# Optimization experiments

Hardware: AMD Instinct MI355X
Metric: run time of the kernel (lower is better)

Reference implementation:

```python
import jax, jax.numpy as jnp
import numpy as np

N = 100_000      # nodes
E = 400_000      # edges
POS = 3          # pos_dim
F = 128          # feats_dim (kernel_dim)
M = 16           # m_dim
FE = 16          # fourier_features
EIN = 2 * F + 2 * FE + 1   # 289 edge mlp input
EHID = 2 * EIN             # 578
NIN = F + M                # 144
NHID = 2 * F               # 256
EPS = 1e-5


def _ln(x, g, b):
    m = x.mean(-1, keepdims=True)
    v = ((x - m) ** 2).mean(-1, keepdims=True)
    return (x - m) * jax.lax.rsqrt(v + EPS) * g + b


def setup_inputs() -> dict:
    key = jax.random.key(0)
    ks = jax.random.split(key, 8)

    def xav(k, i, o):
        return jax.random.normal(k, (i, o), jnp.float32) * np.float32(np.sqrt(2.0 / (i + o)))

    x = jax.random.normal(ks[0], (N, POS + F), jnp.float32)
    edge_index = jax.random.randint(ks[1], (2, E), 0, N, dtype=jnp.int64)
    return {
        "x": x,
        "edge_index": edge_index,
        "e_w1": xav(ks[2], EIN, EHID), "e_b1": jnp.zeros((EHID,), jnp.float32),
        "e_w2": xav(ks[3], EHID, M),   "e_b2": jnp.zeros((M,), jnp.float32),
        "en1_g": jnp.ones((M,), jnp.float32), "en1_b": jnp.zeros((M,), jnp.float32),
        "en2_g": jnp.ones((M,), jnp.float32), "en2_b": jnp.zeros((M,), jnp.float32),
        "nn1_g": jnp.ones((F,), jnp.float32), "nn1_b": jnp.zeros((F,), jnp.float32),
        "n_w1": xav(ks[4], NIN, NHID), "n_b1": jnp.zeros((NHID,), jnp.float32),
        "n_w2": xav(ks[5], NHID, F),   "n_b2": jnp.zeros((F,), jnp.float32),
        "nn2_g": jnp.ones((F,), jnp.float32), "nn2_b": jnp.zeros((F,), jnp.float32),
    }


def reference(x, edge_index, e_w1, e_b1, e_w2, e_b2, en1_g, en1_b, en2_g, en2_b,
              nn1_g, nn1_b, n_w1, n_b1, n_w2, n_b2, nn2_g, nn2_b):
    coors, feats = x[:, :POS], x[:, POS:]
    src, dst = edge_index[0], edge_index[1]  # x_j = feats[src], x_i = feats[dst]

    rel = coors[src] - coors[dst]                      # [E,3]
    d = (rel ** 2).sum(-1, keepdims=True)              # [E,1] squared distance
    scales = jnp.asarray(2.0, jnp.float32) ** jnp.arange(FE)
    ds = d / scales                                    # [E,FE]
    edge_attr = jnp.concatenate([jnp.sin(ds), jnp.cos(ds), d], -1)  # [E,2*FE+1]

    # edge MLP + LayerNorm (message)
    m = jnp.concatenate([feats[dst], feats[src], edge_attr], -1)    # [E,EIN]
    m = jax.nn.silu(m @ e_w1 + e_b1)
    m = jax.nn.silu(m @ e_w2 + e_b2)                                # [E,M]
    m = _ln(m, en1_g, en1_b)

    # scatter-add to target nodes, then LayerNorm
    m_i = jax.ops.segment_sum(m, dst, num_segments=N)               # [N,M]
    m_i = _ln(m_i, en2_g, en2_b)

    # node update MLP with residual
    h = jnp.concatenate([_ln(feats, nn1_g, nn1_b), m_i], -1)        # [N,NIN]
    h = jax.nn.silu(h @ n_w1 + n_b1)
    h = h @ n_w2 + n_b2
    h = _ln(h, nn2_g, nn2_b)
    out = feats + h
    return jnp.concatenate([coors, out], -1)                        # [N,POS+F]
```

## Files before the change

### kernel.cpp

```cpp
#include <hip/hip_runtime.h>
#include <math.h>

#define N_NODES 100000
#define N_EDGES 400000
#define POSD 3
#define F 128
#define M 16
#define EIN 289
#define EHID 578
#define NIN 144
#define NHID 256
#define ROW 131
#define LNEPS 1e-5f

#define KP 320
#define KPA 328
#define NP 640
#define EPB 32
#define NSLICE 10
#define NTW 5
#define HIDP 640
#define HIDPA 648

#define NPB2 80
#define NK1 160
#define NK1P 168
#define NSL2 5
#define NHIDP 264

typedef _Float16 half8 __attribute__((ext_vector_type(8)));
typedef _Float16 half4 __attribute__((ext_vector_type(4)));
typedef float f32x4 __attribute__((ext_vector_type(4)));

__device__ __forceinline__ float silu_f(float v) { return v / (1.f + __expf(-v)); }

__global__ __launch_bounds__(256) void prep_feats(
    const float* __restrict__ x, _Float16* __restrict__ feats)
{
    long long i = (long long)blockIdx.x * 256 + threadIdx.x;
    if (i < (long long)N_NODES * F) {
        int n = (int)(i >> 7), k = (int)(i & 127);
        feats[i] = (_Float16)x[(long long)n * ROW + POSD + k];
    }
}

__global__ __launch_bounds__(256) void prep_weights(
    const float* __restrict__ w1, const float* __restrict__ w2,
    _Float16* __restrict__ w1ks, _Float16* __restrict__ w2t)
{
    long long idx = (long long)blockIdx.x * 256 + threadIdx.x;
    const long long n1 = (long long)NSLICE * NP * 32;
    if (idx < n1) {
        int s   = (int)(idx / (NP * 32));
        int rem = (int)(idx - (long long)s * (NP * 32));
        int c   = rem >> 5;
        int kk  = rem & 31;
        int k   = s * 32 + kk;
        float v = (k < EIN && c < EHID) ? w1[(long long)k * EHID + c] : 0.f;
        w1ks[idx] = (_Float16)v;
    } else {
        long long j = idx - n1;
        if (j < (long long)M * HIDP) {
            int oc = (int)(j / HIDP);
            int k  = (int)(j - (long long)oc * HIDP);
            float v = (k < EHID) ? w2[(long long)k * M + oc] : 0.f;
            w2t[j] = (_Float16)v;
        }
    }
}

__global__ __launch_bounds__(256) void prep_weights_node(
    const float* __restrict__ w1, const float* __restrict__ w2,
    _Float16* __restrict__ w1ks2, _Float16* __restrict__ w2ks)
{
    int idx = blockIdx.x * 256 + threadIdx.x;
    const int n1 = NSL2 * 256 * 32;
    if (idx < n1) {
        int s = idx >> 13, rem = idx & 8191;
        int c = rem >> 5, kk = rem & 31;
        int k = s * 32 + kk;
        w1ks2[idx] = (_Float16)((k < NIN) ? w1[k * NHID + c] : 0.f);
    } else if (idx < n1 + 8 * 128 * 32) {
        int j = idx - n1;
        int s = j >> 12, rem = j & 4095;
        int c = rem >> 5, kk = rem & 31;
        int k = s * 32 + kk;
        w2ks[j] = (_Float16)w2[k * F + c];
    }
}

__global__ __launch_bounds__(512, 4) void edge_kernel(
    const _Float16* __restrict__ feats, const float* __restrict__ x,
    const int* __restrict__ ei,
    const _Float16* __restrict__ w1ks, const float* __restrict__ b1,
    const _Float16* __restrict__ w2t, const float* __restrict__ b2,
    const float* __restrict__ g1, const float* __restrict__ bb1,
    float* __restrict__ m_i)
{
    __shared__ __align__(16) _Float16 smem[EPB * HIDPA];
    _Float16* lds_A = smem;
    _Float16* lds_H = smem;
    __shared__ float part[4][EPB][M];
    __shared__ int   src_s[EPB], dst_s[EPB];
    __shared__ float d_s[EPB];

    const int t    = threadIdx.x;
    const int lane = t & 63;
    const int wv   = t >> 6;
    const int cl16 = lane & 15;
    const int h4   = lane >> 4;
    const long long ebase = (long long)blockIdx.x * EPB;

    if (t < EPB) {
        int s = ei[ebase + t];
        int d = ei[(long long)N_EDGES + ebase + t];
        src_s[t] = s; dst_s[t] = d;
        float dx = x[(long long)s*ROW+0] - x[(long long)d*ROW+0];
        float dy = x[(long long)s*ROW+1] - x[(long long)d*ROW+1];
        float dz = x[(long long)s*ROW+2] - x[(long long)d*ROW+2];
        d_s[t] = dx*dx + dy*dy + dz*dz;
    }
    __syncthreads();

    for (int i = t; i < EPB * 32; i += 512) {
        int row = i >> 5, g = i & 31;
        int node = (g < 16) ? dst_s[row] : src_s[row];
        half8 v = *(const half8*)(feats + (long long)node * F + ((g & 15) << 3));
        *(half8*)(lds_A + row * KPA + (g << 3)) = v;
    }
    for (int i = t; i < EPB * 64; i += 512) {
        int row = i >> 6, j = i & 63;
        float v;
        if (j < 16)       v = __sinf(ldexpf(d_s[row], -j));
        else if (j < 32)  v = __cosf(ldexpf(d_s[row], -(j - 16)));
        else if (j == 32) v = d_s[row];
        else              v = 0.f;
        lds_A[row * KPA + 256 + j] = (_Float16)v;
    }
    __syncthreads();

    f32x4 acc[2][NTW] = {};
    const bool live[NTW] = {
        (wv * NTW + 0) * 16 < EHID, (wv * NTW + 1) * 16 < EHID,
        (wv * NTW + 2) * 16 < EHID, (wv * NTW + 3) * 16 < EHID,
        (wv * NTW + 4) * 16 < EHID };
    #pragma unroll
    for (int s = 0; s < NSLICE; ++s) {
        half8 bf[NTW];
        #pragma unroll
        for (int nt = 0; nt < NTW; ++nt) {
            if (live[nt]) {
                int ntile = wv * NTW + nt;
                bf[nt] = *(const half8*)(w1ks + (long long)s * (NP * 32)
                                         + ntile * 512 + cl16 * 32 + h4 * 8);
            }
        }
        const int G = s * 4 + h4;
        half8 af[2];
        #pragma unroll
        for (int mt = 0; mt < 2; ++mt)
            af[mt] = *(const half8*)(lds_A + (mt * 16 + cl16) * KPA + G * 8);
        #pragma unroll
        for (int nt = 0; nt < NTW; ++nt) {
            if (live[nt]) {
                #pragma unroll
                for (int mt = 0; mt < 2; ++mt)
                    acc[mt][nt] = __builtin_amdgcn_mfma_f32_16x16x32_f16(
                                      af[mt], bf[nt], acc[mt][nt], 0, 0, 0);
            }
        }
    }

    half8 bq[5];
    {
        const int eh = wv & 1;  (void)eh;
        const int kq = wv >> 1;
        const int oc = cl16;
        #pragma unroll
        for (int k5 = 0; k5 < 5; ++k5) {
            int ks = kq * 5 + k5;
            bq[k5] = *(const half8*)(w2t + oc * HIDP + ks * 32 + h4 * 8);
        }
    }
    __syncthreads();

    #pragma unroll
    for (int nt = 0; nt < NTW; ++nt) {
        int hcol = (wv * NTW + nt) * 16 + cl16;
        float bias = (hcol < EHID) ? b1[hcol] : 0.f;
        #pragma unroll
        for (int mt = 0; mt < 2; ++mt) {
            #pragma unroll
            for (int r = 0; r < 4; ++r) {
                int edge = mt * 16 + h4 * 4 + r;
                float v = (hcol < EHID) ? silu_f(acc[mt][nt][r] + bias) : 0.f;
                lds_H[edge * HIDPA + hcol] = (_Float16)v;
            }
        }
    }
    __syncthreads();

    {
        const int eh = wv & 1;
        const int kq = wv >> 1;
        f32x4 acc2 = {};
        const int oc = cl16;
        const int edgeA = eh * 16 + oc;
        #pragma unroll
        for (int k5 = 0; k5 < 5; ++k5) {
            int ks = kq * 5 + k5;
            int G2 = ks * 4 + h4;
            const half8 a = *(const half8*)(lds_H + edgeA * HIDPA + G2 * 8);
            acc2 = __builtin_amdgcn_mfma_f32_16x16x32_f16(a, bq[k5], acc2, 0, 0, 0);
        }
        #pragma unroll
        for (int r = 0; r < 4; ++r)
            part[kq][eh * 16 + h4 * 4 + r][oc] = acc2[r];
    }
    __syncthreads();

    if (wv < 2) {
        const int eh = wv;
        const int oc = cl16;
        float g = g1[oc], bb = bb1[oc], b2v = b2[oc];
        #pragma unroll
        for (int r = 0; r < 4; ++r) {
            int edge = eh * 16 + h4 * 4 + r;
            float v = part[0][edge][oc] + part[1][edge][oc]
                    + part[2][edge][oc] + part[3][edge][oc] + b2v;
            v = silu_f(v);
            float s = v, s2 = v * v;
            #pragma unroll
            for (int m = 8; m >= 1; m >>= 1) {
                s  += __shfl_xor(s,  m, 16);
                s2 += __shfl_xor(s2, m, 16);
            }
            float mean = s * (1.f / 16.f);
            float var  = s2 * (1.f / 16.f) - mean * mean;
            float outv = (v - mean) * rsqrtf(var + LNEPS) * g + bb;
            atomicAdd(&m_i[(long long)dst_s[edge] * M + oc], outv);
        }
    }
}

__global__ __launch_bounds__(512, 4) void node_kernel(
    const _Float16* __restrict__ feats, const float* __restrict__ x,
    const float* __restrict__ m_i,
    const float* __restrict__ en2g, const float* __restrict__ en2b,
    const float* __restrict__ nn1g, const float* __restrict__ nn1b,
    const _Float16* __restrict__ w1ks2, const float* __restrict__ b1,
    const _Float16* __restrict__ w2ks, const float* __restrict__ b2,
    const float* __restrict__ nn2g, const float* __restrict__ nn2b,
    float* __restrict__ out)
{
    __shared__ __align__(16) _Float16 smem[NPB2 * NHIDP];
    _Float16* lds_A = smem;
    _Float16* lds_H = smem;
    __shared__ float rsum2[NPB2], rsq2[NPB2];

    const int t    = threadIdx.x;
    const int lane = t & 63;
    const int wv   = t >> 6;
    const int cl16 = lane & 15;
    const int h4   = lane >> 4;
    const long long nb = (long long)blockIdx.x * NPB2;

    if (t < NPB2) { rsum2[t] = 0.f; rsq2[t] = 0.f; }

    #pragma unroll
    for (int p = 0; p < 5; ++p) {
        int nl = p * 16 + (t >> 5);
        int l  = t & 31;
        half4 v4 = *(const half4*)(feats + (nb + nl) * F + l * 4);
        float v[4]; float s = 0.f, s2 = 0.f;
        #pragma unroll
        for (int i = 0; i < 4; ++i) {
            v[i] = (float)v4[i]; s += v[i]; s2 += v[i]*v[i];
        }
        #pragma unroll
        for (int m = 16; m >= 1; m >>= 1) {
            s  += __shfl_xor(s,  m, 32);
            s2 += __shfl_xor(s2, m, 32);
        }
        float mean = s * (1.f/128.f);
        float var  = s2 * (1.f/128.f) - mean*mean;
        float rs   = rsqrtf(var + LNEPS);
        half4 w;
        #pragma unroll
        for (int i = 0; i < 4; ++i) {
            int c = l * 4 + i;
            w[i] = (_Float16)((v[i] - mean) * rs * nn1g[c] + nn1b[c]);
        }
        *(half4*)(lds_A + nl * NK1P + l * 4) = w;
    }
    for (int i = t; i < NPB2 * M; i += 512) {
        int nl = i >> 4, oc = i & 15;
        float v = m_i[(nb + nl) * M + oc];
        float a = v, a2 = v * v;
        #pragma unroll
        for (int m = 8; m >= 1; m >>= 1) {
            a  += __shfl_xor(a,  m, 16);
            a2 += __shfl_xor(a2, m, 16);
        }
        float mn = a * (1.f/16.f);
        float vr = a2 * (1.f/16.f) - mn*mn;
        float lv = (v - mn) * rsqrtf(vr + LNEPS) * en2g[oc] + en2b[oc];
        lds_A[nl * NK1P + 128 + oc] = (_Float16)lv;
    }
    for (int i = t; i < NPB2 * 16; i += 512) {
        int nl = i >> 4, j = i & 15;
        lds_A[nl * NK1P + 144 + j] = (_Float16)0.f;
    }
    __syncthreads();

    f32x4 acc[5][2] = {};
    #pragma unroll
    for (int s = 0; s < NSL2; ++s) {
        half8 bf[2];
        #pragma unroll
        for (int nt = 0; nt < 2; ++nt) {
            int ntile = wv * 2 + nt;
            bf[nt] = *(const half8*)(w1ks2 + s * (NHID * 32)
                                     + ntile * 512 + cl16 * 32 + h4 * 8);
        }
        const int G = s * 4 + h4;
        half8 af[5];
        #pragma unroll
        for (int mt = 0; mt < 5; ++mt)
            af[mt] = *(const half8*)(lds_A + (mt * 16 + cl16) * NK1P + G * 8);
        #pragma unroll
        for (int nt = 0; nt < 2; ++nt) {
            #pragma unroll
            for (int mt = 0; mt < 5; ++mt)
                acc[mt][nt] = __builtin_amdgcn_mfma_f32_16x16x32_f16(
                                  af[mt], bf[nt], acc[mt][nt], 0, 0, 0);
        }
    }
    __syncthreads();

    #pragma unroll
    for (int nt = 0; nt < 2; ++nt) {
        int hcol = (wv * 2 + nt) * 16 + cl16;
        float bias = b1[hcol];
        #pragma unroll
        for (int mt = 0; mt < 5; ++mt) {
            #pragma unroll
            for (int r = 0; r < 4; ++r) {
                int row = mt * 16 + h4 * 4 + r;
                float v = silu_f(acc[mt][nt][r] + bias);
                lds_H[row * NHIDP + hcol] = (_Float16)v;
            }
        }
    }
    __syncthreads();

    f32x4 acc2[5] = {};
    const int col = wv * 16 + cl16;
    #pragma unroll
    for (int s = 0; s < 8; ++s) {
        const half8 b = *(const half8*)(w2ks + s * (F * 32) + col * 32 + h4 * 8);
        const int G2 = s * 4 + h4;
        #pragma unroll
        for (int mt = 0; mt < 5; ++mt) {
            int row = mt * 16 + cl16;
            const half8 a = *(const half8*)(lds_H + row * NHIDP + G2 * 8);
            acc2[mt] = __builtin_amdgcn_mfma_f32_16x16x32_f16(a, b, acc2[mt], 0, 0, 0);
        }
    }

    float y[5][4];
    float b2v = b2[col];
    #pragma unroll
    for (int mt = 0; mt < 5; ++mt) {
        #pragma unroll
        for (int r = 0; r < 4; ++r) {
            float v = acc2[mt][r] + b2v;
            y[mt][r] = v;
            float s = v, s2 = v * v;
            #pragma unroll
            for (int m = 8; m >= 1; m >>= 1) {
                s  += __shfl_xor(s,  m, 16);
                s2 += __shfl_xor(s2, m, 16);
            }
            if (cl16 == 0) {
                int row = mt * 16 + h4 * 4 + r;
                atomicAdd(&rsum2[row], s);
                atomicAdd(&rsq2[row],  s2);
            }
        }
    }
    __syncthreads();

    float gcol2 = nn2g[col], bcol2 = nn2b[col];
    #pragma unroll
    for (int mt = 0; mt < 5; ++mt) {
        #pragma unroll
        for (int r = 0; r < 4; ++r) {
            int row = mt * 16 + h4 * 4 + r;
            long long node = nb + row;
            float mn = rsum2[row] * (1.f/128.f);
            float vr = rsq2[row] * (1.f/128.f) - mn*mn;
            float rs = rsqrtf(vr + LNEPS);
            float res = x[node * ROW + POSD + col];
            out[node * ROW + POSD + col] = res + (y[mt][r] - mn) * rs * gcol2 + bcol2;
        }
    }
    for (int i = t; i < NPB2 * POSD; i += 512) {
        int nl = i / 3, c = i - nl * 3;
        long long node = nb + nl;
        out[node * ROW + c] = x[node * ROW + c];
    }
}

extern "C" void kernel_launch(void* const* d_in, const int* in_sizes, int n_in,
                              void* d_out, int out_size, void* d_ws, size_t ws_size,
                              hipStream_t stream) {
    const float* x    = (const float*)d_in[0];
    const int*   ei   = (const int*)d_in[1];
    const float* e_w1 = (const float*)d_in[2];
    const float* e_b1 = (const float*)d_in[3];
    const float* e_w2 = (const float*)d_in[4];
    const float* e_b2 = (const float*)d_in[5];
    const float* en1g = (const float*)d_in[6];
    const float* en1b = (const float*)d_in[7];
    const float* en2g = (const float*)d_in[8];
    const float* en2b = (const float*)d_in[9];
    const float* nn1g = (const float*)d_in[10];
    const float* nn1b = (const float*)d_in[11];
    const float* n_w1 = (const float*)d_in[12];
    const float* n_b1 = (const float*)d_in[13];
    const float* n_w2 = (const float*)d_in[14];
    const float* n_b2 = (const float*)d_in[15];
    const float* nn2g = (const float*)d_in[16];
    const float* nn2b = (const float*)d_in[17];
    float* out = (float*)d_out;

    char* ws = (char*)d_ws;
    float*    m_i   = (float*)ws;
    _Float16* w1ks  = (_Float16*)(ws + 6400000);
    _Float16* w2t   = (_Float16*)(ws + 6809600);
    _Float16* feats = (_Float16*)(ws + 6830080);
    _Float16* w1ks2 = (_Float16*)(ws + 32430080);
    _Float16* w2ks  = (_Float16*)(ws + 32512000);

    hipMemsetAsync(m_i, 0, (size_t)N_NODES * M * sizeof(float), stream);
    prep_weights<<<840, 256, 0, stream>>>(e_w1, e_w2, w1ks, w2t);
    prep_weights_node<<<288, 256, 0, stream>>>(n_w1, n_w2, w1ks2, w2ks);
    prep_feats<<<(N_NODES * F + 255) / 256, 256, 0, stream>>>(x, feats);
    edge_kernel<<<N_EDGES / EPB, 512, 0, stream>>>(
        feats, x, ei, w1ks, e_b1, w2t, e_b2, en1g, en1b, m_i);
    node_kernel<<<N_NODES / NPB2, 512, 0, stream>>>(
        feats, x, m_i, en2g, en2b, nn1g, nn1b, w1ks2, n_b1, w2ks, n_b2, nn2g, nn2b, out);
}
```

Measured before the change: 512.4 us.

## Precompute per-node first-layer projections and gather them per edge

Splits the first edge-MLP layer by linearity: the feats[dst] and feats[src] parts of W1 are multiplied once per node into Pd/Ps tables (N x 584 fp16). The edge kernel then gathers these rows, adds the RBF-term matmul, the bias and silu, which cuts edge GEMM work from 10 K-slices to 2. The cost is extra global traffic: two 584-wide fp16 gathers per edge plus writing roughly 234 MB of tables. The path is only taken when the workspace is large enough, otherwise the old kernel runs. Also switches silu to a hardware reciprocal.

```diff
diff --git a/kernel.cpp b/kernel.cpp
--- a/kernel.cpp
+++ b/kernel.cpp
@@ -23,16 +23,30 @@
 #define HIDPA 648
 
 #define NPB2 80
-#define NK1 160
 #define NK1P 168
 #define NSL2 5
 #define NHIDP 264
 
+#define PSTR 584
+#define ARBF_STR 72
+
+#define WS_W1KS   6400000
+#define WS_W2T    6809600
+#define WS_FEATS  6830080
+#define WS_W1KS2  32430080
+#define WS_W2KS   32512000
+#define WS_B1H    32577536
+#define WS_PD     33554432LL
+#define WS_PS     (WS_PD + 116800000LL + 4096LL)
+#define WS_FAST_NEED (WS_PS + 116800000LL + 4096LL)
+
 typedef _Float16 half8 __attribute__((ext_vector_type(8)));
 typedef _Float16 half4 __attribute__((ext_vector_type(4)));
 typedef float f32x4 __attribute__((ext_vector_type(4)));
 
-__device__ __forceinline__ float silu_f(float v) { return v / (1.f + __expf(-v)); }
+__device__ __forceinline__ float silu_f(float v) {
+    return v * __builtin_amdgcn_rcpf(1.f + __expf(-v));
+}
 
 __global__ __launch_bounds__(256) void prep_feats(
     const float* __restrict__ x, _Float16* __restrict__ feats)
@@ -46,10 +60,13 @@
 
 __global__ __launch_bounds__(256) void prep_weights(
     const float* __restrict__ w1, const float* __restrict__ w2,
-    _Float16* __restrict__ w1ks, _Float16* __restrict__ w2t)
+    const float* __restrict__ b1,
+    _Float16* __restrict__ w1ks, _Float16* __restrict__ w2t,
+    _Float16* __restrict__ b1h)
 {
     long long idx = (long long)blockIdx.x * 256 + threadIdx.x;
     const long long n1 = (long long)NSLICE * NP * 32;
+    const long long n2 = n1 + (long long)M * HIDP;
     if (idx < n1) {
         int s   = (int)(idx / (NP * 32));
         int rem = (int)(idx - (long long)s * (NP * 32));
@@ -58,14 +75,15 @@
         int k   = s * 32 + kk;
         float v = (k < EIN && c < EHID) ? w1[(long long)k * EHID + c] : 0.f;
         w1ks[idx] = (_Float16)v;
-    } else {
+    } else if (idx < n2) {
         long long j = idx - n1;
-        if (j < (long long)M * HIDP) {
-            int oc = (int)(j / HIDP);
-            int k  = (int)(j - (long long)oc * HIDP);
-            float v = (k < EHID) ? w2[(long long)k * M + oc] : 0.f;
-            w2t[j] = (_Float16)v;
-        }
+        int oc = (int)(j / HIDP);
+        int k  = (int)(j - (long long)oc * HIDP);
+        float v = (k < EHID) ? w2[(long long)k * M + oc] : 0.f;
+        w2t[j] = (_Float16)v;
+    } else if (idx < n2 + HIDP) {
+        int j = (int)(idx - n2);
+        b1h[j] = (_Float16)((j < EHID) ? b1[j] : 0.f);
     }
 }
 
@@ -89,7 +107,223 @@
     }
 }
 
-__global__ __launch_bounds__(512, 4) void edge_kernel(
+__global__ __launch_bounds__(512, 2) void prep_pdps(
+    const _Float16* __restrict__ feats, const _Float16* __restrict__ w1ks,
+    _Float16* __restrict__ Pd, _Float16* __restrict__ Ps)
+{
+    const int t = threadIdx.x;
+    const int lane = t & 63, wv = t >> 6, cl16 = lane & 15, h4 = lane >> 4;
+    const long long nb = (long long)blockIdx.x * NPB2;
+    const bool live[5] = {
+        (wv * 5 + 0) * 16 < EHID, (wv * 5 + 1) * 16 < EHID,
+        (wv * 5 + 2) * 16 < EHID, (wv * 5 + 3) * 16 < EHID,
+        (wv * 5 + 4) * 16 < EHID };
+
+    #pragma unroll
+    for (int hf = 0; hf < 2; ++hf) {
+        _Float16* P = hf ? Ps : Pd;
+        f32x4 acc[5][5] = {};
+        #pragma unroll
+        for (int s = 0; s < 4; ++s) {
+            half8 bf[5];
+            #pragma unroll
+            for (int nt = 0; nt < 5; ++nt)
+                if (live[nt])
+                    bf[nt] = *(const half8*)(w1ks + (long long)(hf * 4 + s) * (NP * 32)
+                                             + (wv * 5 + nt) * 512 + cl16 * 32 + h4 * 8);
+            half8 af[5];
+            #pragma unroll
+            for (int mt = 0; mt < 5; ++mt)
+                af[mt] = *(const half8*)(feats + (nb + mt * 16 + cl16) * F + s * 32 + h4 * 8);
+            #pragma unroll
+            for (int nt = 0; nt < 5; ++nt)
+                if (live[nt]) {
+                    #pragma unroll
+                    for (int mt = 0; mt < 5; ++mt)
+                        acc[mt][nt] = __builtin_amdgcn_mfma_f32_16x16x32_f16(
+                                          af[mt], bf[nt], acc[mt][nt], 0, 0, 0);
+                }
+        }
+        #pragma unroll
+        for (int nt = 0; nt < 5; ++nt) {
+            if (!live[nt]) continue;
+            int hcol = (wv * 5 + nt) * 16 + cl16;
+            if (hcol < PSTR) {
+                #pragma unroll
+                for (int mt = 0; mt < 5; ++mt) {
+                    #pragma unroll
+                    for (int r = 0; r < 4; ++r) {
+                        int row = mt * 16 + h4 * 4 + r;
+                        P[(nb + row) * PSTR + hcol] = (_Float16)acc[mt][nt][r];
+                    }
+                }
+            }
+        }
+    }
+}
+
+__global__ __launch_bounds__(512, 4) void edge_fast(
+    const float* __restrict__ x, const int* __restrict__ ei,
+    const _Float16* __restrict__ w1ks, const _Float16* __restrict__ b1h,
+    const _Float16* __restrict__ w2t, const float* __restrict__ b2,
+    const float* __restrict__ g1, const float* __restrict__ bb1,
+    float* __restrict__ m_i,
+    const _Float16* __restrict__ Pd, const _Float16* __restrict__ Ps)
+{
+    __shared__ __align__(16) _Float16 lds_H[EPB * HIDPA];
+    __shared__ __align__(16) char ubuf[8192];
+    __shared__ int   src_s[EPB], dst_s[EPB];
+    __shared__ float d_s[EPB];
+    _Float16* A_rbf = (_Float16*)ubuf;
+    float (*part)[EPB][M] = (float (*)[EPB][M])ubuf;
+
+    const int t    = threadIdx.x;
+    const int lane = t & 63;
+    const int wv   = t >> 6;
+    const int cl16 = lane & 15;
+    const int h4   = lane >> 4;
+    const long long ebase = (long long)blockIdx.x * EPB;
+
+    if (t < EPB) {
+        int s = ei[ebase + t];
+        int d = ei[(long long)N_EDGES + ebase + t];
+        src_s[t] = s; dst_s[t] = d;
+        float dx = x[(long long)s*ROW+0] - x[(long long)d*ROW+0];
+        float dy = x[(long long)s*ROW+1] - x[(long long)d*ROW+1];
+        float dz = x[(long long)s*ROW+2] - x[(long long)d*ROW+2];
+        d_s[t] = dx*dx + dy*dy + dz*dz;
+    }
+    __syncthreads();
+
+    for (int i = t; i < EPB * 64; i += 512) {
+        int row = i >> 6, j = i & 63;
+        float dv = d_s[row];
+        float ds = ldexpf(dv, -(j & 15));
+        float v = (j < 16) ? __sinf(ds) : (j < 32) ? __cosf(ds)
+                : (j == 32) ? dv : 0.f;
+        A_rbf[row * ARBF_STR + j] = (_Float16)v;
+    }
+    __syncthreads();
+
+    f32x4 acc[2][NTW] = {};
+    const bool live[NTW] = {
+        (wv * NTW + 0) * 16 < EHID, (wv * NTW + 1) * 16 < EHID,
+        (wv * NTW + 2) * 16 < EHID, (wv * NTW + 3) * 16 < EHID,
+        (wv * NTW + 4) * 16 < EHID };
+    #pragma unroll
+    for (int s = 0; s < 2; ++s) {
+        half8 bf[NTW];
+        #pragma unroll
+        for (int nt = 0; nt < NTW; ++nt)
+            if (live[nt])
+                bf[nt] = *(const half8*)(w1ks + (long long)(8 + s) * (NP * 32)
+                                         + (wv * NTW + nt) * 512 + cl16 * 32 + h4 * 8);
+        #pragma unroll
+        for (int mt = 0; mt < 2; ++mt) {
+            const half8 af = *(const half8*)(A_rbf + (mt * 16 + cl16) * ARBF_STR
+                                             + s * 32 + h4 * 8);
+            #pragma unroll
+            for (int nt = 0; nt < NTW; ++nt)
+                if (live[nt])
+                    acc[mt][nt] = __builtin_amdgcn_mfma_f32_16x16x32_f16(
+                                      af, bf[nt], acc[mt][nt], 0, 0, 0);
+        }
+    }
+
+    half8 bq[5];
+    {
+        const int kq = wv >> 1;
+        #pragma unroll
+        for (int k5 = 0; k5 < 5; ++k5)
+            bq[k5] = *(const half8*)(w2t + cl16 * HIDP + (kq * 5 + k5) * 32 + h4 * 8);
+    }
+    half8 pd8[5], ps8[5];
+    #pragma unroll
+    for (int p = 0; p < 5; ++p) {
+        int i5 = t + p * 512;
+        int e  = i5 / 80;
+        int g  = i5 - e * 80;
+        pd8[p] = *(const half8*)(Pd + (long long)dst_s[e] * PSTR + g * 8);
+        ps8[p] = *(const half8*)(Ps + (long long)src_s[e] * PSTR + g * 8);
+    }
+
+    #pragma unroll
+    for (int nt = 0; nt < NTW; ++nt) {
+        if (!live[nt]) continue;
+        int hcol = (wv * NTW + nt) * 16 + cl16;
+        #pragma unroll
+        for (int mt = 0; mt < 2; ++mt) {
+            #pragma unroll
+            for (int r = 0; r < 4; ++r) {
+                int edge = mt * 16 + h4 * 4 + r;
+                lds_H[edge * HIDPA + hcol] = (_Float16)acc[mt][nt][r];
+            }
+        }
+    }
+    __syncthreads();
+
+    #pragma unroll
+    for (int p = 0; p < 5; ++p) {
+        int i5 = t + p * 512;
+        int e  = i5 / 80;
+        int g  = i5 - e * 80;
+        half8 rb = *(const half8*)(lds_H + e * HIDPA + g * 8);
+        half8 bb = *(const half8*)(b1h + g * 8);
+        half8 o;
+        #pragma unroll
+        for (int j = 0; j < 8; ++j) {
+            int h = g * 8 + j;
+            float v = (float)pd8[p][j] + (float)ps8[p][j]
+                    + (float)rb[j] + (float)bb[j];
+            o[j] = (h < EHID) ? (_Float16)silu_f(v) : (_Float16)0.f;
+        }
+        *(half8*)(lds_H + e * HIDPA + g * 8) = o;
+    }
+    __syncthreads();
+
+    {
+        const int eh = wv & 1;
+        const int kq = wv >> 1;
+        f32x4 acc2 = {};
+        const int oc = cl16;
+        const int edgeA = eh * 16 + oc;
+        #pragma unroll
+        for (int k5 = 0; k5 < 5; ++k5) {
+            int G2 = (kq * 5 + k5) * 4 + h4;
+            const half8 a = *(const half8*)(lds_H + edgeA * HIDPA + G2 * 8);
+            acc2 = __builtin_amdgcn_mfma_f32_16x16x32_f16(a, bq[k5], acc2, 0, 0, 0);
+        }
+        #pragma unroll
+        for (int r = 0; r < 4; ++r)
+            part[kq][eh * 16 + h4 * 4 + r][cl16] = acc2[r];
+    }
+    __syncthreads();
+
+    if (wv < 2) {
+        const int eh = wv;
+        const int oc = cl16;
+        float g = g1[oc], bb = bb1[oc], b2v = b2[oc];
+        #pragma unroll
+        for (int r = 0; r < 4; ++r) {
+            int edge = eh * 16 + h4 * 4 + r;
+            float v = part[0][edge][oc] + part[1][edge][oc]
+                    + part[2][edge][oc] + part[3][edge][oc] + b2v;
+            v = silu_f(v);
+            float s = v, s2 = v * v;
+            #pragma unroll
+            for (int m = 8; m >= 1; m >>= 1) {
+                s  += __shfl_xor(s,  m, 16);
+                s2 += __shfl_xor(s2, m, 16);
+            }
+            float mean = s * (1.f / 16.f);
+            float var  = s2 * (1.f / 16.f) - mean * mean;
+            float outv = (v - mean) * rsqrtf(var + LNEPS) * g + bb;
+            atomicAdd(&m_i[(long long)dst_s[edge] * M + oc], outv);
+        }
+    }
+}
+
+__global__ __launch_bounds__(512, 4) void edge_fused(
     const _Float16* __restrict__ feats, const float* __restrict__ x,
     const int* __restrict__ ei,
     const _Float16* __restrict__ w1ks, const float* __restrict__ b1,
@@ -130,11 +364,10 @@
     }
     for (int i = t; i < EPB * 64; i += 512) {
         int row = i >> 6, j = i & 63;
-        float v;
-        if (j < 16)       v = __sinf(ldexpf(d_s[row], -j));
-        else if (j < 32)  v = __cosf(ldexpf(d_s[row], -(j - 16)));
-        else if (j == 32) v = d_s[row];
-        else              v = 0.f;
+        float dv = d_s[row];
+        float ds = ldexpf(dv, -(j & 15));
+        float v = (j < 16) ? __sinf(ds) : (j < 32) ? __cosf(ds)
+                : (j == 32) ? dv : 0.f;
         lds_A[row * KPA + 256 + j] = (_Float16)v;
     }
     __syncthreads();
@@ -148,39 +381,31 @@
     for (int s = 0; s < NSLICE; ++s) {
         half8 bf[NTW];
         #pragma unroll
-        for (int nt = 0; nt < NTW; ++nt) {
-            if (live[nt]) {
-                int ntile = wv * NTW + nt;
+        for (int nt = 0; nt < NTW; ++nt)
+            if (live[nt])
                 bf[nt] = *(const half8*)(w1ks + (long long)s * (NP * 32)
-                                         + ntile * 512 + cl16 * 32 + h4 * 8);
-            }
-        }
+                                         + (wv * NTW + nt) * 512 + cl16 * 32 + h4 * 8);
         const int G = s * 4 + h4;
         half8 af[2];
         #pragma unroll
         for (int mt = 0; mt < 2; ++mt)
             af[mt] = *(const half8*)(lds_A + (mt * 16 + cl16) * KPA + G * 8);
         #pragma unroll
-        for (int nt = 0; nt < NTW; ++nt) {
+        for (int nt = 0; nt < NTW; ++nt)
             if (live[nt]) {
                 #pragma unroll
                 for (int mt = 0; mt < 2; ++mt)
                     acc[mt][nt] = __builtin_amdgcn_mfma_f32_16x16x32_f16(
                                       af[mt], bf[nt], acc[mt][nt], 0, 0, 0);
             }
-        }
     }
 
     half8 bq[5];
     {
-        const int eh = wv & 1;  (void)eh;
         const int kq = wv >> 1;
-        const int oc = cl16;
-        #pragma unroll
-        for (int k5 = 0; k5 < 5; ++k5) {
-            int ks = kq * 5 + k5;
-            bq[k5] = *(const half8*)(w2t + oc * HIDP + ks * 32 + h4 * 8);
-        }
+        #pragma unroll
+        for (int k5 = 0; k5 < 5; ++k5)
+            bq[k5] = *(const half8*)(w2t + cl16 * HIDP + (kq * 5 + k5) * 32 + h4 * 8);
     }
     __syncthreads();
 
@@ -208,8 +433,7 @@
         const int edgeA = eh * 16 + oc;
         #pragma unroll
         for (int k5 = 0; k5 < 5; ++k5) {
-            int ks = kq * 5 + k5;
-            int G2 = ks * 4 + h4;
+            int G2 = (kq * 5 + k5) * 4 + h4;
             const half8 a = *(const half8*)(lds_H + edgeA * HIDPA + G2 * 8);
             acc2 = __builtin_amdgcn_mfma_f32_16x16x32_f16(a, bq[k5], acc2, 0, 0, 0);
         }
@@ -318,11 +542,9 @@
     for (int s = 0; s < NSL2; ++s) {
         half8 bf[2];
         #pragma unroll
-        for (int nt = 0; nt < 2; ++nt) {
-            int ntile = wv * 2 + nt;
+        for (int nt = 0; nt < 2; ++nt)
             bf[nt] = *(const half8*)(w1ks2 + s * (NHID * 32)
-                                     + ntile * 512 + cl16 * 32 + h4 * 8);
-        }
+                                     + (wv * 2 + nt) * 512 + cl16 * 32 + h4 * 8);
         const int G = s * 4 + h4;
         half8 af[5];
         #pragma unroll
@@ -437,18 +659,30 @@
 
     char* ws = (char*)d_ws;
     float*    m_i   = (float*)ws;
-    _Float16* w1ks  = (_Float16*)(ws + 6400000);
-    _Float16* w2t   = (_Float16*)(ws + 6809600);
-    _Float16* feats = (_Float16*)(ws + 6830080);
-    _Float16* w1ks2 = (_Float16*)(ws + 32430080);
-    _Float16* w2ks  = (_Float16*)(ws + 32512000);
+    _Float16* w1ks  = (_Float16*)(ws + WS_W1KS);
+    _Float16* w2t   = (_Float16*)(ws + WS_W2T);
+    _Float16* feats = (_Float16*)(ws + WS_FEATS);
+    _Float16* w1ks2 = (_Float16*)(ws + WS_W1KS2);
+    _Float16* w2ks  = (_Float16*)(ws + WS_W2KS);
+    _Float16* b1h   = (_Float16*)(ws + WS_B1H);
+    _Float16* Pd    = (_Float16*)(ws + WS_PD);
+    _Float16* Ps    = (_Float16*)(ws + WS_PS);
+
+    const bool fast = ws_size >= (size_t)WS_FAST_NEED;
 
     hipMemsetAsync(m_i, 0, (size_t)N_NODES * M * sizeof(float), stream);
-    prep_weights<<<840, 256, 0, stream>>>(e_w1, e_w2, w1ks, w2t);
+    prep_weights<<<843, 256, 0, stream>>>(e_w1, e_w2, e_b1, w1ks, w2t, b1h);
     prep_weights_node<<<288, 256, 0, stream>>>(n_w1, n_w2, w1ks2, w2ks);
     prep_feats<<<(N_NODES * F + 255) / 256, 256, 0, stream>>>(x, feats);
-    edge_kernel<<<N_EDGES / EPB, 512, 0, stream>>>(
-        feats, x, ei, w1ks, e_b1, w2t, e_b2, en1g, en1b, m_i);
+
+    if (fast) {
+        prep_pdps<<<N_NODES / NPB2, 512, 0, stream>>>(feats, w1ks, Pd, Ps);
+        edge_fast<<<N_EDGES / EPB, 512, 0, stream>>>(
+            x, ei, w1ks, b1h, w2t, e_b2, en1g, en1b, m_i, Pd, Ps);
+    } else {
+        edge_fused<<<N_EDGES / EPB, 512, 0, stream>>>(
+            feats, x, ei, w1ks, e_b1, w2t, e_b2, en1g, en1b, m_i);
+    }
     node_kernel<<<N_NODES / NPB2, 512, 0, stream>>>(
         feats, x, m_i, en2g, en2b, nn1g, nn1b, w1ks2, n_b1, w2ks, n_b2, nn2g, nn2b, out);
 }
```

Measured after the change: 543.6 us. 6.1% more time.
